# Performance work log

Hardware: AMD Instinct MI355X
Metric: run time of the kernel (lower is better)

The kernel has to match this reference:

```python
import jax, jax.numpy as jnp
import numpy as np

B, T, C, H, N = 4, 4096, 2048, 32, 64
DMIX, DDEC = 32, 64
N_LAYER, LAYER_ID = 24, 12
GN_EPS = 1e-5 * 8.0 ** 2  # eps = 1e-5 * head_size_divisor**2


def setup_inputs() -> dict:
    key = jax.random.key(0)
    ks = jax.random.split(key, 24)
    r01 = LAYER_ID / (N_LAYER - 1)
    r1a0 = 1.0 - LAYER_ID / N_LAYER
    ddd = (np.arange(C, dtype=np.float32) / C).reshape(1, 1, C)
    maa = lambda p: jnp.asarray(1.0 - ddd ** p, dtype=jnp.float32)
    # decay speed schedule (canonical RWKV6, over channel dim)
    n = np.arange(C, dtype=np.float32)
    decay = (-6.0 + 5.0 * (n / (C - 1)) ** (0.7 + 1.3 * r01)).reshape(1, 1, C)
    # time_faaaa zigzag schedule
    m = np.arange(C, dtype=np.float32)
    zig = ((m + 1) % 3 - 1) * 0.1
    faaaa = (r01 * (1 - m / (C - 1)) + zig).reshape(H, N)
    s = 1.0 / np.sqrt(C)
    return {
        "x": jax.random.normal(ks[0], (B, T, C), jnp.float32),
        "shift_state": jax.random.normal(ks[1], (B, C), jnp.float32),
        "wkv_state": jnp.zeros((B, H, N, N), jnp.float32),
        "time_maa_x": maa(r1a0),
        "time_maa_w": maa(r1a0),
        "time_maa_k": maa(r1a0),
        "time_maa_v": jnp.asarray(1.0 - (ddd ** r1a0 + 0.3 * r01), jnp.float32),
        "time_maa_r": maa(0.5 * r1a0),
        "time_maa_g": maa(0.5 * r1a0),
        "time_maa_w1": jax.random.normal(ks[2], (C, 5 * DMIX), jnp.float32) * 0.01,
        "time_maa_w2": jax.random.uniform(ks[3], (5, DMIX, C), jnp.float32, -0.01, 0.01),
        "time_decay": jnp.asarray(decay, jnp.float32),
        "time_decay_w1": jax.random.normal(ks[4], (C, DDEC), jnp.float32) * 0.01,
        "time_decay_w2": jax.random.uniform(ks[5], (DDEC, C), jnp.float32, -0.01, 0.01),
        "time_faaaa": jnp.asarray(faaaa, jnp.float32),
        "Wr": jax.random.normal(ks[6], (C, C), jnp.float32) * s,
        "Wk": jax.random.normal(ks[7], (C, C), jnp.float32) * s,
        "Wv": jax.random.normal(ks[8], (C, C), jnp.float32) * s,
        "Wg": jax.random.normal(ks[9], (C, C), jnp.float32) * s,
        "Wo": jax.random.normal(ks[10], (C, C), jnp.float32) * s,
        "gn_weight": jnp.ones((C,), jnp.float32),
        "gn_bias": jnp.zeros((C,), jnp.float32),
    }


def reference(x, shift_state, wkv_state, time_maa_x, time_maa_w, time_maa_k,
              time_maa_v, time_maa_r, time_maa_g, time_maa_w1, time_maa_w2,
              time_decay, time_decay_w1, time_decay_w2, time_faaaa,
              Wr, Wk, Wv, Wg, Wo, gn_weight, gn_bias):
    b, t, c = x.shape
    # token shift: previous token (seeded by shift_state) minus current
    xx = jnp.concatenate([shift_state[:, None, :], x[:, :-1]], axis=1) - x
    lx = x[:, -1]
    # LoRA token-shift mixing
    xxx = x + xx * time_maa_x
    t5 = jnp.tanh(xxx @ time_maa_w1).reshape(b, t, 5, DMIX)
    mixes = jnp.einsum('btfd,fdc->fbtc', t5, time_maa_w2)
    mw, mk, mv, mr, mg = mixes
    xw = x + xx * (time_maa_w + mw)
    xk = x + xx * (time_maa_k + mk)
    xv = x + xx * (time_maa_v + mv)
    xr = x + xx * (time_maa_r + mr)
    xg = x + xx * (time_maa_g + mg)
    r = xr @ Wr
    k = xk @ Wk
    v = xv @ Wv
    g = jax.nn.silu(xg @ Wg)
    # data-dependent decay via LoRA; wkv6 uses log-decay -exp(w)
    w = time_decay + jnp.tanh(xw @ time_decay_w1) @ time_decay_w2
    glog = -jnp.exp(w)  # [b,t,c]
    to_heads = lambda z: z.reshape(b, t, H, N).transpose(1, 0, 2, 3)  # [t,b,h,n]
    rh, kh, vh, gh = to_heads(r), to_heads(k), to_heads(v), to_heads(glog)
    u = time_faaaa  # [H,N]

    def step(S, inp):
        r_t, k_t, v_t, g_t = inp  # each [b,h,n]
        kv = jnp.einsum('bhk,bhv->bhkv', k_t, v_t)
        o_t = jnp.einsum('bhk,bhkv->bhv', r_t, S + u[None, :, :, None] * kv)
        S = jnp.exp(g_t)[..., None] * S + kv
        return S, o_t

    state, o = jax.lax.scan(step, wkv_state, (rh, kh, vh, gh))
    o = o.transpose(1, 0, 2, 3).reshape(b, t, c)  # [b,t,c]
    # GroupNorm with H groups over channel dim
    og = o.reshape(b, t, H, N)
    mu = og.mean(-1, keepdims=True)
    var = og.var(-1, keepdims=True)
    on = (og - mu) * jax.lax.rsqrt(var + GN_EPS)
    on = on * gn_weight.reshape(H, N) + gn_bias.reshape(H, N)
    out = (on.reshape(b, t, c) * g) @ Wo
    return out, lx, state
```

## Files before the change

kernel.cpp:

```cpp
#include <hip/hip_runtime.h>
#include <hip/hip_bf16.h>
#include <stdint.h>

#define DEV __device__ __forceinline__

typedef __bf16 bf16x8 __attribute__((ext_vector_type(8)));
typedef float f32x4 __attribute__((ext_vector_type(4)));
typedef unsigned short u16x8 __attribute__((ext_vector_type(8)));

constexpr int kB = 4, kT = 4096, kC = 2048, kH = 32, kN = 64;
constexpr int kM = kB * kT;
constexpr int SEGN = 8, TSEG = kT / SEGN, CHN = TSEG / 64;

DEV float bfu2f(unsigned short u) {
  union { uint32_t i; float f; } x; x.i = ((uint32_t)u) << 16; return x.f;
}
DEV unsigned short f2bfu(float f) {
  union { float f; uint32_t i; } x; x.f = f;
  uint32_t r = x.i + 0x7FFFu + ((x.i >> 16) & 1u);
  return (unsigned short)(r >> 16);
}

DEV void gld16(const void* g, void* l) {
  __builtin_amdgcn_global_load_lds(
      (const __attribute__((address_space(1))) void*)g,
      (__attribute__((address_space(3))) void*)l, 16, 0, 0);
}

DEV int swzb(int row, int byteoff) { return (row << 7) + (byteoff ^ ((row & 7) << 4)); }
DEV int swz64(int row, int byteoff) { return (row << 6) + (byteoff ^ ((row & 3) << 4)); }

__global__ __launch_bounds__(256) void trans_bf16(
    const float* __restrict__ in, unsigned short* __restrict__ out, int R, int Cn) {
  __shared__ __attribute__((aligned(16))) unsigned short tile[64][65];
  const int t = threadIdx.x;
  const int r0 = blockIdx.y * 64, c0 = blockIdx.x * 64;
  const int lr = t >> 6, lc = t & 63;
#pragma unroll
  for (int i = 0; i < 16; i++) {
    int rr = lr + i * 4;
    int gr = r0 + rr, gc = c0 + lc;
    if (gr < R && gc < Cn) tile[rr][lc] = f2bfu(in[(size_t)gr * Cn + gc]);
  }
  __syncthreads();
#pragma unroll
  for (int i = 0; i < 16; i++) {
    int cc = lr + i * 4;
    int gc = c0 + cc, gr = r0 + lc;
    if (gc < Cn && gr < R) out[(size_t)gc * R + gr] = tile[lc][cc];
  }
}

__global__ __launch_bounds__(256) void prep_x2(
    const float* __restrict__ x, const float* __restrict__ shift,
    const float* __restrict__ maax,
    unsigned short* __restrict__ xxx, float* __restrict__ lx) {
  size_t i4 = ((size_t)blockIdx.x * 256 + threadIdx.x) * 4;
  int c = (int)(i4 & (kC - 1));
  size_t bt = i4 >> 11;
  int tt = (int)(bt & (kT - 1));
  int b = (int)(bt >> 12);
  float4 xv = *(const float4*)(x + i4);
  float4 pv = (tt == 0) ? *(const float4*)(shift + (size_t)b * kC + c)
                        : *(const float4*)(x + i4 - kC);
  float4 mx = *(const float4*)(maax + c);
  ushort4 o4;
  o4.x = f2bfu(xv.x + (pv.x - xv.x) * mx.x);
  o4.y = f2bfu(xv.y + (pv.y - xv.y) * mx.y);
  o4.z = f2bfu(xv.z + (pv.z - xv.z) * mx.z);
  o4.w = f2bfu(xv.w + (pv.w - xv.w) * mx.w);
  *(ushort4*)(xxx + i4) = o4;
  if (tt == kT - 1) *(float4*)(lx + (size_t)b * kC + c) = xv;
}

enum { E_F32 = 0, E_BF16 = 1, E_TANH = 2, E_SILU = 3, E_DECAY = 4 };

template <int BM, int BN, int EPI>
__global__ __launch_bounds__(256) void gemm_k(
    const unsigned short* __restrict__ A, const unsigned short* __restrict__ Bt,
    void* __restrict__ Cout, const float* __restrict__ aux, int M, int N, int K) {
  constexpr int WGM = (BM == 128 && BN == 128) ? 2 : (BM == 64 ? 2 : 4);
  constexpr int WGN = 4 / WGM;
  constexpr int WM = BM / WGM, WN = BN / WGN;
  constexpr int WR = WM / 16, WC = WN / 16;
  __shared__ __attribute__((aligned(16))) unsigned short As[BM * 32];
  __shared__ __attribute__((aligned(16))) unsigned short Bs[BN * 32];
  const int t = threadIdx.x, wid = t >> 6, l = t & 63;
  const int m0 = blockIdx.x * BM, n0 = blockIdx.y * BN;
  const int wm0 = (wid / WGN) * WM, wn0 = (wid % WGN) * WN;
  f32x4 acc[WR][WC];
#pragma unroll
  for (int i = 0; i < WR; i++)
#pragma unroll
    for (int j = 0; j < WC; j++) acc[i][j] = f32x4{0.f, 0.f, 0.f, 0.f};

  const int rowS = t >> 2, cbS = (t & 3) * 16;
  const char* Ab = (const char*)A;
  const char* Bb = (const char*)Bt;
  const int aoff = (wm0 + (l & 15)) * 32 + (l >> 4) * 8;
  const int boff = (wn0 + (l & 15)) * 32 + (l >> 4) * 8;

  for (int kt = 0; kt < K; kt += 32) {
#pragma unroll
    for (int ia = 0; ia < BM / 64; ia++)
      gld16(Ab + ((size_t)(m0 + ia * 64 + rowS) * K + kt) * 2 + cbS,
            (char*)As + ia * 4096 + wid * 1024);
    if constexpr (BN >= 64) {
#pragma unroll
      for (int ib = 0; ib < BN / 64; ib++)
        gld16(Bb + ((size_t)(n0 + ib * 64 + rowS) * K + kt) * 2 + cbS,
              (char*)Bs + ib * 4096 + wid * 1024);
    } else {
      if (t < BN * 4)
        gld16(Bb + ((size_t)(n0 + rowS) * K + kt) * 2 + cbS,
              (char*)Bs + wid * 1024);
    }
    __syncthreads();
    bf16x8 af[WR], bfv[WC];
#pragma unroll
    for (int mi = 0; mi < WR; mi++) af[mi] = *(const bf16x8*)(&As[aoff + mi * 512]);
#pragma unroll
    for (int ni = 0; ni < WC; ni++) bfv[ni] = *(const bf16x8*)(&Bs[boff + ni * 512]);
#pragma unroll
    for (int mi = 0; mi < WR; mi++)
#pragma unroll
      for (int ni = 0; ni < WC; ni++)
        acc[mi][ni] = __builtin_amdgcn_mfma_f32_16x16x32_bf16(af[mi], bfv[ni], acc[mi][ni], 0, 0, 0);
    __syncthreads();
  }

#pragma unroll
  for (int mi = 0; mi < WR; mi++) {
#pragma unroll
    for (int ni = 0; ni < WC; ni++) {
      int row = m0 + wm0 + mi * 16 + (l >> 4) * 4;
      int col = n0 + wn0 + ni * 16 + (l & 15);
#pragma unroll
      for (int j = 0; j < 4; j++) {
        float v = acc[mi][ni][j];
        size_t idx = (size_t)(row + j) * N + col;
        if constexpr (EPI == E_F32) ((float*)Cout)[idx] = v;
        else if constexpr (EPI == E_BF16) ((unsigned short*)Cout)[idx] = f2bfu(v);
        else if constexpr (EPI == E_TANH) ((unsigned short*)Cout)[idx] = f2bfu(tanhf(v));
        else if constexpr (EPI == E_SILU) ((unsigned short*)Cout)[idx] = f2bfu(v / (1.f + expf(-v)));
        else if constexpr (EPI == E_DECAY) {
          float w = v + aux[col];
          ((float*)Cout)[idx] = expf(-expf(w));
        }
      }
    }
  }
}

template <int EPI>
__global__ __launch_bounds__(512, 2) void gemm256_k(
    const unsigned short* __restrict__ A, const unsigned short* __restrict__ Bt,
    void* __restrict__ Cout, int M, int N, int K) {
  extern __shared__ __attribute__((aligned(16))) char lds[];
  const int tid = threadIdx.x, wid = tid >> 6, l = tid & 63;
  const int fr = l & 15, fq = l >> 4;

  const int mtiles = M >> 8, ntiles = N >> 8;
  const int slab = mtiles >> 3;
  const int xcd = blockIdx.x & 7, loc = blockIdx.x >> 3;
  const int m0 = (xcd * slab + loc / ntiles) * 256;
  const int n0 = (loc % ntiles) * 256;

  const int wm = (wid >> 2) * 128, wn = (wid & 3) * 64;

  const int srow0 = tid >> 2;
  const int scb = ((tid & 3) * 16) ^ ((srow0 & 3) << 4);
  const char* pa2[2]; const char* pb2[2];
#pragma unroll
  for (int i = 0; i < 2; i++) {
    pa2[i] = (const char*)A + (size_t)(m0 + i * 128 + srow0) * K * 2 + scb;
    pb2[i] = (const char*)Bt + (size_t)(n0 + i * 128 + srow0) * K * 2 + scb;
  }

  const char* vA[8]; const char* vB[4];
#pragma unroll
  for (int mi = 0; mi < 8; mi++)
    vA[mi] = lds + swz64(wm + mi * 16 + fr, fq * 16);
#pragma unroll
  for (int ni = 0; ni < 4; ni++)
    vB[ni] = lds + 32768 + swz64(wn + ni * 16 + fr, fq * 16);

  f32x4 acc[8][4];
#pragma unroll
  for (int i = 0; i < 8; i++)
#pragma unroll
    for (int j = 0; j < 4; j++) acc[i][j] = f32x4{0.f, 0.f, 0.f, 0.f};

  auto STG = [&](int q, int s, int ktb) {
    const int d = q * 65536 + s * 16384 + wid * 1024;
    gld16(pa2[0] + ktb + s * 64, lds + d);
    gld16(pa2[1] + ktb + s * 64, lds + d + 8192);
    gld16(pb2[0] + ktb + s * 64, lds + 32768 + d);
    gld16(pb2[1] + ktb + s * 64, lds + 32768 + d + 8192);
  };

  auto PH = [&](int p, int s, bool doStage, int ktbNext, int vm) {
// ... 3 lines not shown
      asm volatile("s_waitcnt vmcnt(0)" ::: "memory");
    __builtin_amdgcn_s_barrier();
    __builtin_amdgcn_sched_barrier(0);
    const int pb = p * 65536 + s * 16384;
    bf16x8 a[8], b[4];
#pragma unroll
    for (int mi = 0; mi < 8; mi++) a[mi] = *(const bf16x8*)(vA[mi] + pb);
#pragma unroll
    for (int ni = 0; ni < 4; ni++) b[ni] = *(const bf16x8*)(vB[ni] + pb);
    if (doStage) STG(p ^ 1, s, ktbNext);
    __builtin_amdgcn_sched_barrier(0);
    __builtin_amdgcn_s_setprio(1);
#pragma unroll
    for (int ni = 0; ni < 4; ni++)
#pragma unroll
      for (int mi = 0; mi < 8; mi++)
        acc[mi][ni] = __builtin_amdgcn_mfma_f32_16x16x32_bf16(a[mi], b[ni], acc[mi][ni], 0, 0, 0);
    __builtin_amdgcn_s_setprio(0);
  };

  const int KT = K >> 6;
  STG(0, 0, 0);
  STG(0, 1, 0);

  int T = 0;
  for (; T + 2 < KT; T += 2) {
    PH(0, 0, true, (T + 1) * 128, 4);
    PH(0, 1, true, (T + 1) * 128, 4);
    PH(1, 0, true, (T + 2) * 128, 4);
    PH(1, 1, true, (T + 2) * 128, 4);
  }
  PH(0, 0, true, (KT - 1) * 128, 4);
  PH(0, 1, true, (KT - 1) * 128, 4);
  PH(1, 0, false, 0, 4);
  PH(1, 1, false, 0, 0);

#pragma unroll
  for (int mi = 0; mi < 8; mi++)
#pragma unroll
    for (int ni = 0; ni < 4; ni++) {
      int row = m0 + wm + mi * 16 + fq * 4;
      int col = n0 + wn + ni * 16 + fr;
#pragma unroll
      for (int j = 0; j < 4; j++) {
        float v = acc[mi][ni][j];
        size_t idx = (size_t)(row + j) * N + col;
        if constexpr (EPI == E_F32) ((float*)Cout)[idx] = v;
        else if constexpr (EPI == E_BF16) ((unsigned short*)Cout)[idx] = f2bfu(v);
        else if constexpr (EPI == E_SILU) ((unsigned short*)Cout)[idx] = f2bfu(v / (1.f + expf(-v)));
      }
    }
}

__global__ __launch_bounds__(256) void mix2f_k(
    const unsigned short* __restrict__ t5, const unsigned short* __restrict__ w2t,
    const float* __restrict__ x, const float* __restrict__ shift,
    const float* __restrict__ maa1, const float* __restrict__ maa2,
    unsigned short* __restrict__ xo1, unsigned short* __restrict__ xo2,
    int f1, int f2) {
  __shared__ __attribute__((aligned(16))) unsigned short As1[64 * 32];
  __shared__ __attribute__((aligned(16))) unsigned short Bs1[64 * 32];
  __shared__ __attribute__((aligned(16))) unsigned short As2[64 * 32];
  __shared__ __attribute__((aligned(16))) unsigned short Bs2[64 * 32];
  const int t = threadIdx.x, wid = t >> 6, l = t & 63;
  const int m0 = blockIdx.x * 64, n0 = blockIdx.y * 64;
  const int wm0 = (wid >> 1) * 32, wn0 = (wid & 1) * 32;
  const int rowS = t >> 2, cbS = (t & 3) * 16;
  const int aoff = (wm0 + (l & 15)) * 32 + (l >> 4) * 8;
  const int boff = (wn0 + (l & 15)) * 32 + (l >> 4) * 8;

  gld16((const char*)t5 + ((size_t)(m0 + rowS) * 160 + f1 * 32) * 2 + cbS, (char*)As1 + wid * 1024);
  gld16((const char*)w2t + ((size_t)(n0 + rowS) * 160 + f1 * 32) * 2 + cbS, (char*)Bs1 + wid * 1024);
  gld16((const char*)t5 + ((size_t)(m0 + rowS) * 160 + f2 * 32) * 2 + cbS, (char*)As2 + wid * 1024);
  gld16((const char*)w2t + ((size_t)(n0 + rowS) * 160 + f2 * 32) * 2 + cbS, (char*)Bs2 + wid * 1024);
  __syncthreads();
  bf16x8 a10 = *(const bf16x8*)(&As1[aoff]), a11 = *(const bf16x8*)(&As1[aoff + 512]);
  bf16x8 b10 = *(const bf16x8*)(&Bs1[boff]), b11 = *(const bf16x8*)(&Bs1[boff + 512]);
  bf16x8 a20 = *(const bf16x8*)(&As2[aoff]), a21 = *(const bf16x8*)(&As2[aoff + 512]);
  bf16x8 b20 = *(const bf16x8*)(&Bs2[boff]), b21 = *(const bf16x8*)(&Bs2[boff + 512]);
  f32x4 ac1[2][2], ac2[2][2];
#pragma unroll
  for (int i = 0; i < 2; i++)
#pragma unroll
    for (int j = 0; j < 2; j++) { ac1[i][j] = f32x4{0.f, 0.f, 0.f, 0.f}; ac2[i][j] = f32x4{0.f, 0.f, 0.f, 0.f}; }
  ac1[0][0] = __builtin_amdgcn_mfma_f32_16x16x32_bf16(a10, b10, ac1[0][0], 0, 0, 0);
  ac1[0][1] = __builtin_amdgcn_mfma_f32_16x16x32_bf16(a10, b11, ac1[0][1], 0, 0, 0);
  ac1[1][0] = __builtin_amdgcn_mfma_f32_16x16x32_bf16(a11, b10, ac1[1][0], 0, 0, 0);
  ac1[1][1] = __builtin_amdgcn_mfma_f32_16x16x32_bf16(a11, b11, ac1[1][1], 0, 0, 0);
  ac2[0][0] = __builtin_amdgcn_mfma_f32_16x16x32_bf16(a20, b20, ac2[0][0], 0, 0, 0);
  ac2[0][1] = __builtin_amdgcn_mfma_f32_16x16x32_bf16(a20, b21, ac2[0][1], 0, 0, 0);
  ac2[1][0] = __builtin_amdgcn_mfma_f32_16x16x32_bf16(a21, b20, ac2[1][0], 0, 0, 0);
  ac2[1][1] = __builtin_amdgcn_mfma_f32_16x16x32_bf16(a21, b21, ac2[1][1], 0, 0, 0);

#pragma unroll
  for (int mi = 0; mi < 2; mi++)
#pragma unroll
    for (int ni = 0; ni < 2; ni++) {
      int row = m0 + wm0 + mi * 16 + (l >> 4) * 4;
      int col = n0 + wn0 + ni * 16 + (l & 15);
      float mv1 = maa1[col], mv2 = maa2[col];
#pragma unroll
      for (int j = 0; j < 4; j++) {
        int rrow = row + j;
        int tt = rrow & (kT - 1);
        size_t idx = (size_t)rrow * kC + col;
        float xv = x[idx];
        float pv = (tt == 0) ? shift[(size_t)(rrow >> 12) * kC + col] : x[idx - kC];
        float d = pv - xv;
        xo1[idx] = f2bfu(xv + d * (mv1 + ac1[mi][ni][j]));
        xo2[idx] = f2bfu(xv + d * (mv2 + ac2[mi][ni][j]));
      }
    }
}

__global__ __launch_bounds__(256) void mixf_k(
    const unsigned short* __restrict__ t5, const unsigned short* __restrict__ w2t,
    const float* __restrict__ x, const float* __restrict__ shift,
    const float* __restrict__ maa, unsigned short* __restrict__ xout, int f) {
  __shared__ __attribute__((aligned(16))) unsigned short As[64 * 32];
  __shared__ __attribute__((aligned(16))) unsigned short Bs[64 * 32];
  const int t = threadIdx.x, wid = t >> 6, l = t & 63;
  const int m0 = blockIdx.x * 64, n0 = blockIdx.y * 64;
  const int wm0 = (wid >> 1) * 32, wn0 = (wid & 1) * 32;
  const int rowS = t >> 2, cbS = (t & 3) * 16;
  const int aoff = (wm0 + (l & 15)) * 32 + (l >> 4) * 8;
  const int boff = (wn0 + (l & 15)) * 32 + (l >> 4) * 8;

  gld16((const char*)t5 + ((size_t)(m0 + rowS) * 160 + f * 32) * 2 + cbS, (char*)As + wid * 1024);
  gld16((const char*)w2t + ((size_t)(n0 + rowS) * 160 + f * 32) * 2 + cbS, (char*)Bs + wid * 1024);
  __syncthreads();
  bf16x8 a0 = *(const bf16x8*)(&As[aoff]), a1 = *(const bf16x8*)(&As[aoff + 512]);
  bf16x8 b0 = *(const bf16x8*)(&Bs[boff]), b1 = *(const bf16x8*)(&Bs[boff + 512]);
  f32x4 acc[2][2];
  acc[0][0] = f32x4{0.f, 0.f, 0.f, 0.f}; acc[0][1] = f32x4{0.f, 0.f, 0.f, 0.f};
  acc[1][0] = f32x4{0.f, 0.f, 0.f, 0.f}; acc[1][1] = f32x4{0.f, 0.f, 0.f, 0.f};
  acc[0][0] = __builtin_amdgcn_mfma_f32_16x16x32_bf16(a0, b0, acc[0][0], 0, 0, 0);
  acc[0][1] = __builtin_amdgcn_mfma_f32_16x16x32_bf16(a0, b1, acc[0][1], 0, 0, 0);
  acc[1][0] = __builtin_amdgcn_mfma_f32_16x16x32_bf16(a1, b0, acc[1][0], 0, 0, 0);
  acc[1][1] = __builtin_amdgcn_mfma_f32_16x16x32_bf16(a1, b1, acc[1][1], 0, 0, 0);

#pragma unroll
  for (int mi = 0; mi < 2; mi++)
#pragma unroll
    for (int ni = 0; ni < 2; ni++) {
      int row = m0 + wm0 + mi * 16 + (l >> 4) * 4;
      int col = n0 + wn0 + ni * 16 + (l & 15);
      float mv = maa[col];
#pragma unroll
      for (int j = 0; j < 4; j++) {
        int rrow = row + j;
        int tt = rrow & (kT - 1);
        size_t idx = (size_t)rrow * kC + col;
        float xv = x[idx];
        float pv = (tt == 0) ? shift[(size_t)(rrow >> 12) * kC + col] : x[idx - kC];
        xout[idx] = f2bfu(xv + (pv - xv) * (mv + acc[mi][ni][j]));
      }
    }
}

__global__ __launch_bounds__(256) void wkv_local_k(
    const unsigned short* __restrict__ kb, const unsigned short* __restrict__ vb,
    const float* __restrict__ ed, float* __restrict__ Lbuf, float* __restrict__ Dseg) {
  const int bid = blockIdx.x;
  const int bh = bid >> 3, seg = bid & 7;
  const int h = bh & 31, b = bh >> 5;
  const int tid = threadIdx.x, w = tid >> 6, l = tid & 63;
  __shared__ __attribute__((aligned(16))) unsigned short KQks[4096];
  __shared__ __attribute__((aligned(16))) unsigned short Vt[4096];
  __shared__ float segp[4][64];
  __shared__ float DLs[64];

  const int fr = l & 15, fq = l >> 4;
  f32x4 Sreg[4];
#pragma unroll
  for (int ni = 0; ni < 4; ni++) Sreg[ni] = f32x4{0.f, 0.f, 0.f, 0.f};

  float dtot = 1.f;
  float kv[16], dv[16], vv[16];
  {
    size_t g = ((size_t)b * kT + seg * TSEG + w * 16) * kC + h * 64 + l;
#pragma unroll
    for (int i = 0; i < 16; i++) {
      kv[i] = bfu2f(kb[g]); vv[i] = bfu2f(vb[g]); dv[i] = ed[g];
      g += kC;
    }
  }

  for (int ch = 0; ch < CHN; ++ch) {
    float p = 1.f;
#pragma unroll
    for (int i = 0; i < 16; i++) p *= dv[i];
    segp[w][l] = p;
    __syncthreads();
    float pre = 1.f;
    if (w > 0) pre *= segp[0][l];
    if (w > 1) pre *= segp[1][l];
    if (w > 2) pre *= segp[2][l];
    if (w == 3) DLs[l] = pre * p;

    unsigned short kqrow[16], vtrow[16];
    float run = pre;
#pragma unroll
    for (int i = 0; i < 16; i++) {
      run *= dv[i];
      kqrow[i] = f2bfu(kv[i] / run);
      vtrow[i] = f2bfu(vv[i]);
    }
    {
      u16x8 q0, q1, v0, v1;
#pragma unroll
      for (int j = 0; j < 8; j++) { q0[j] = kqrow[j]; q1[j] = kqrow[j + 8]; v0[j] = vtrow[j]; v1[j] = vtrow[j + 8]; }
      *(u16x8*)((char*)KQks + swzb(l, w * 32)) = q0;
      *(u16x8*)((char*)KQks + swzb(l, w * 32 + 16)) = q1;
      *(u16x8*)((char*)Vt + swzb(l, w * 32)) = v0;
      *(u16x8*)((char*)Vt + swzb(l, w * 32 + 16)) = v1;
    }
    if (ch < CHN - 1) {
      size_t g = ((size_t)b * kT + seg * TSEG + (ch + 1) * 64 + w * 16) * kC + h * 64 + l;
#pragma unroll
      for (int i = 0; i < 16; i++) {
        kv[i] = bfu2f(kb[g]); vv[i] = bfu2f(vb[g]); dv[i] = ed[g];
        g += kC;
      }
    }
    __syncthreads();

    bf16x8 kA0 = *(const bf16x8*)((const char*)KQks + swzb(w * 16 + fr, fq * 16));
    bf16x8 kA1 = *(const bf16x8*)((const char*)KQks + swzb(w * 16 + fr, fq * 16 + 64));
    f32x4 kvacc[4];
#pragma unroll
    for (int ni = 0; ni < 4; ni++) {
      bf16x8 bv0 = *(const bf16x8*)((const char*)Vt + swzb(ni * 16 + fr, fq * 16));
      bf16x8 bv1 = *(const bf16x8*)((const char*)Vt + swzb(ni * 16 + fr, fq * 16 + 64));
      kvacc[ni] = __builtin_amdgcn_mfma_f32_16x16x32_bf16(kA0, bv0, f32x4{0.f, 0.f, 0.f, 0.f}, 0, 0, 0);
      kvacc[ni] = __builtin_amdgcn_mfma_f32_16x16x32_bf16(kA1, bv1, kvacc[ni], 0, 0, 0);
    }
    float dlj[4];
#pragma unroll
    for (int j = 0; j < 4; j++) dlj[j] = DLs[w * 16 + fq * 4 + j];
#pragma unroll
    for (int ni = 0; ni < 4; ni++)
#pragma unroll
      for (int j = 0; j < 4; j++)
        Sreg[ni][j] = (Sreg[ni][j] + kvacc[ni][j]) * dlj[j];
    dtot *= DLs[l];
    __syncthreads();
  }

  float* Lp = Lbuf + (size_t)bid * 4096;
#pragma unroll
  for (int ni = 0; ni < 4; ni++)
#pragma unroll
    for (int j = 0; j < 4; j++)
      Lp[(size_t)(w * 16 + fq * 4 + j) * 64 + ni * 16 + fr] = Sreg[ni][j];
  if (w == 0) Dseg[(size_t)bid * 64 + l] = dtot;
}

__global__ __launch_bounds__(256) void wkv_combine_k(
    const float* __restrict__ s0, const float* __restrict__ Dseg,
    float* __restrict__ Lbuf, float* __restrict__ sOut) {
  const int bh = blockIdx.x, tid = threadIdx.x;
  const int k = tid >> 2, v0 = (tid & 3) * 16;
  float4 s[4];
  const float* sp = s0 + (size_t)bh * 4096 + (size_t)k * 64 + v0;
#pragma unroll
  for (int q = 0; q < 4; q++) s[q] = ((const float4*)sp)[q];
  for (int seg = 0; seg < SEGN; ++seg) {
    size_t idx = (size_t)bh * SEGN + seg;
    float d = Dseg[idx * 64 + k];
    float* Lp = Lbuf + idx * 4096 + (size_t)k * 64 + v0;
#pragma unroll
    for (int q = 0; q < 4; q++) {
      float4 lq = ((float4*)Lp)[q];
      ((float4*)Lp)[q] = s[q];
      s[q].x = d * s[q].x + lq.x; s[q].y = d * s[q].y + lq.y;
      s[q].z = d * s[q].z + lq.z; s[q].w = d * s[q].w + lq.w;
    }
  }
  float* op = sOut + (size_t)bh * 4096 + (size_t)k * 64 + v0;
#pragma unroll
  for (int q = 0; q < 4; q++) ((float4*)op)[q] = s[q];
}

__global__ __launch_bounds__(256) void wkv_seg_k(
    const unsigned short* __restrict__ rb, const unsigned short* __restrict__ kb,
    const unsigned short* __restrict__ vb, const float* __restrict__ ed,
    const float* __restrict__ uf, const float* __restrict__ Sini,
    unsigned short* __restrict__ o) {
  const int bid = blockIdx.x;
  const int bh = bid >> 3, seg = bid & 7;
  const int h = bh & 31, b = bh >> 5;
  const int tid = threadIdx.x, w = tid >> 6, l = tid & 63;
  __shared__ __attribute__((aligned(16))) unsigned short RQ[4096];
  __shared__ __attribute__((aligned(16))) unsigned short KQsk[4096];
  __shared__ __attribute__((aligned(16))) unsigned short KQks[4096];
  __shared__ __attribute__((aligned(16))) unsigned short Vt[4096];
  __shared__ __attribute__((aligned(16))) unsigned short Pl[4096];
  __shared__ __attribute__((aligned(16))) unsigned short S0T[4096];
  __shared__ __attribute__((aligned(16))) unsigned short RU[4096];
// ... 95 lines not shown
    }
    float dg[4];
#pragma unroll
    for (int j = 0; j < 4; j++) dg[j] = __shfl(dacc[j], fq * 20 + j, 64);
#pragma unroll
    for (int ni = 0; ni < 4; ni++)
#pragma unroll
      for (int j = 0; j < 4; j++) {
        int row = w * 16 + fq * 4 + j, col = ni * 16 + fr;
        float pv = pacc[ni][j];
        pv = (col < row) ? pv : ((col == row) ? dg[j] : 0.f);
        *(unsigned short*)((char*)Pl + swzb(row, col * 2)) = f2bfu(pv);
      }
    __syncthreads();

    bf16x8 pA0 = *(const bf16x8*)((const char*)Pl + swzb(w * 16 + fr, fq * 16));
    bf16x8 pA1 = *(const bf16x8*)((const char*)Pl + swzb(w * 16 + fr, fq * 16 + 64));
    bf16x8 kA0 = *(const bf16x8*)((const char*)KQks + swzb(w * 16 + fr, fq * 16));
    bf16x8 kA1 = *(const bf16x8*)((const char*)KQks + swzb(w * 16 + fr, fq * 16 + 64));
    f32x4 oacc[4], kvacc[4];
#pragma unroll
    for (int ni = 0; ni < 4; ni++) {
      bf16x8 bv0 = *(const bf16x8*)((const char*)Vt + swzb(ni * 16 + fr, fq * 16));
      bf16x8 bv1 = *(const bf16x8*)((const char*)Vt + swzb(ni * 16 + fr, fq * 16 + 64));
      bf16x8 bs0 = *(const bf16x8*)((const char*)S0T + swzb(ni * 16 + fr, fq * 16));
      bf16x8 bs1 = *(const bf16x8*)((const char*)S0T + swzb(ni * 16 + fr, fq * 16 + 64));
      oacc[ni] = __builtin_amdgcn_mfma_f32_16x16x32_bf16(pA0, bv0, f32x4{0.f, 0.f, 0.f, 0.f}, 0, 0, 0);
      oacc[ni] = __builtin_amdgcn_mfma_f32_16x16x32_bf16(pA1, bv1, oacc[ni], 0, 0, 0);
      oacc[ni] = __builtin_amdgcn_mfma_f32_16x16x32_bf16(a0, bs0, oacc[ni], 0, 0, 0);
      oacc[ni] = __builtin_amdgcn_mfma_f32_16x16x32_bf16(a1, bs1, oacc[ni], 0, 0, 0);
      kvacc[ni] = __builtin_amdgcn_mfma_f32_16x16x32_bf16(kA0, bv0, f32x4{0.f, 0.f, 0.f, 0.f}, 0, 0, 0);
      kvacc[ni] = __builtin_amdgcn_mfma_f32_16x16x32_bf16(kA1, bv1, kvacc[ni], 0, 0, 0);
    }
    size_t obase = ((size_t)b * kT + seg * TSEG + ch * 64) * kC + h * 64;
#pragma unroll
    for (int ni = 0; ni < 4; ni++)
#pragma unroll
      for (int j = 0; j < 4; j++)
        o[obase + (size_t)(w * 16 + fq * 4 + j) * kC + ni * 16 + fr] = f2bfu(oacc[ni][j]);
    __syncthreads();

    float dlj[4];
#pragma unroll
    for (int j = 0; j < 4; j++) dlj[j] = DLs[w * 16 + fq * 4 + j];
#pragma unroll
    for (int ni = 0; ni < 4; ni++)
#pragma unroll
      for (int j = 0; j < 4; j++) {
        int kk2 = w * 16 + fq * 4 + j, vv2 = ni * 16 + fr;
        float sn = (Sreg[ni][j] + kvacc[ni][j]) * dlj[j];
        Sreg[ni][j] = sn;
        *(unsigned short*)((char*)S0T + swzb(vv2, kk2 * 2)) = f2bfu(sn);
      }
    __syncthreads();
  }
}

__global__ __launch_bounds__(256) void gn_k(
    const unsigned short* __restrict__ o, const unsigned short* __restrict__ gb,
    const float* __restrict__ gnw, const float* __restrict__ gnb,
    unsigned short* __restrict__ y) {
  int gi = blockIdx.x * 4 + (threadIdx.x >> 6);
  int j = threadIdx.x & 63;
  int bt = gi >> 5, h = gi & 31;
  size_t idx = (size_t)bt * kC + h * 64 + j;
  float val = bfu2f(o[idx]);
  float s = val, s2 = val * val;
#pragma unroll
  for (int m = 1; m < 64; m <<= 1) {
    s += __shfl_xor(s, m, 64);
    s2 += __shfl_xor(s2, m, 64);
  }
  float mu = s * 0.015625f;
  float var = s2 * 0.015625f - mu * mu;
  float rs = rsqrtf(var + 6.4e-4f);
  float on = (val - mu) * rs * gnw[h * 64 + j] + gnb[h * 64 + j];
  y[idx] = f2bfu(on * bfu2f(gb[idx]));
}

constexpr size_t SZW     = (size_t)2048 * 2048 * 2;
constexpr size_t OFF_WRT = 0;
constexpr size_t OFF_WKT = 1 * SZW;
constexpr size_t OFF_WVT = 2 * SZW;
constexpr size_t OFF_WGT = 3 * SZW;
constexpr size_t OFF_WOT = 4 * SZW;
constexpr size_t OFF_W1T = 5 * SZW;
constexpr size_t OFF_W2T = OFF_W1T + (size_t)160 * 2048 * 2;
constexpr size_t OFF_TD1 = OFF_W2T + (size_t)2048 * 160 * 2;
constexpr size_t OFF_TD2 = OFF_TD1 + (size_t)64 * 2048 * 2;
constexpr size_t OFF_T5  = OFF_TD2 + (size_t)2048 * 64 * 2;
constexpr size_t OFF_DT  = OFF_T5 + (size_t)kM * 160 * 2;
constexpr size_t OFF_EDEC= OFF_DT + (size_t)kM * 64 * 2;
constexpr size_t OFF_XMIX= OFF_EDEC + (size_t)kM * kC * 4;
constexpr size_t OFF_R   = OFF_XMIX + (size_t)kM * kC * 2;
constexpr size_t OFF_K   = OFF_R + (size_t)kM * kC * 2;
constexpr size_t OFF_V   = OFF_K + (size_t)kM * kC * 2;
constexpr size_t OFF_L   = OFF_WRT;

extern "C" void kernel_launch(void* const* d_in, const int* in_sizes, int n_in,
                              void* d_out, int out_size, void* d_ws, size_t ws_size,
                              hipStream_t stream) {
  const float* x     = (const float*)d_in[0];
  const float* shift = (const float*)d_in[1];
  const float* s0    = (const float*)d_in[2];
  const float* maax  = (const float*)d_in[3];
  const float* maaw  = (const float*)d_in[4];
  const float* maak  = (const float*)d_in[5];
  const float* maav  = (const float*)d_in[6];
  const float* maar  = (const float*)d_in[7];
  const float* maag  = (const float*)d_in[8];
  const float* w1    = (const float*)d_in[9];
  const float* w2    = (const float*)d_in[10];
  const float* tdec  = (const float*)d_in[11];
  const float* tdw1  = (const float*)d_in[12];
  const float* tdw2  = (const float*)d_in[13];
  const float* faaaa = (const float*)d_in[14];
  const float* Wr    = (const float*)d_in[15];
  const float* Wk    = (const float*)d_in[16];
  const float* Wv    = (const float*)d_in[17];
  const float* Wg    = (const float*)d_in[18];
  const float* Wo    = (const float*)d_in[19];
  const float* gnw   = (const float*)d_in[20];
  const float* gnb   = (const float*)d_in[21];

  char* ws = (char*)d_ws;
  unsigned short* Wrt  = (unsigned short*)(ws + OFF_WRT);
  unsigned short* Wkt  = (unsigned short*)(ws + OFF_WKT);
  unsigned short* Wvt  = (unsigned short*)(ws + OFF_WVT);
  unsigned short* Wgt  = (unsigned short*)(ws + OFF_WGT);
  unsigned short* Wot  = (unsigned short*)(ws + OFF_WOT);
  unsigned short* w1t  = (unsigned short*)(ws + OFF_W1T);
  unsigned short* w2t  = (unsigned short*)(ws + OFF_W2T);
  unsigned short* td1t = (unsigned short*)(ws + OFF_TD1);
  unsigned short* td2t = (unsigned short*)(ws + OFF_TD2);
  unsigned short* t5   = (unsigned short*)(ws + OFF_T5);
  unsigned short* dtmp = (unsigned short*)(ws + OFF_DT);
  float*          edec = (float*)(ws + OFF_EDEC);
  unsigned short* xg   = (unsigned short*)(ws + OFF_EDEC);
  unsigned short* bufX = (unsigned short*)(ws + OFF_XMIX);
  unsigned short* bufR = (unsigned short*)(ws + OFF_R);
  unsigned short* bufK = (unsigned short*)(ws + OFF_K);
  unsigned short* bufV = (unsigned short*)(ws + OFF_V);
  float*          Lbuf = (float*)(ws + OFF_L);
  float*          DsegP= (float*)(ws + OFF_TD1);

  float* outp  = (float*)d_out;
  float* lx    = outp + (size_t)kM * kC;
  float* stOut = lx + (size_t)kB * kC;

  dim3 blk(256);

  trans_bf16<<<dim3(32, 32), blk, 0, stream>>>(Wr, Wrt, 2048, 2048);
  trans_bf16<<<dim3(32, 32), blk, 0, stream>>>(Wk, Wkt, 2048, 2048);
  trans_bf16<<<dim3(32, 32), blk, 0, stream>>>(Wv, Wvt, 2048, 2048);
  trans_bf16<<<dim3(32, 32), blk, 0, stream>>>(Wg, Wgt, 2048, 2048);
  trans_bf16<<<dim3(32, 32), blk, 0, stream>>>(Wo, Wot, 2048, 2048);
  trans_bf16<<<dim3(3, 32), blk, 0, stream>>>(w1, w1t, 2048, 160);
  trans_bf16<<<dim3(1, 32), blk, 0, stream>>>(tdw1, td1t, 2048, 64);
  trans_bf16<<<dim3(32, 1), blk, 0, stream>>>(tdw2, td2t, 64, 2048);
  trans_bf16<<<dim3(32, 3), blk, 0, stream>>>(w2, w2t, 160, 2048);

  prep_x2<<<dim3(kM * kC / 4 / 256), blk, 0, stream>>>(x, shift, maax, bufX, lx);

  gemm_k<128, 32, E_TANH><<<dim3(kM / 128, 5), blk, 0, stream>>>(bufX, w1t, t5, nullptr, kM, 160, 2048);

  dim3 mgrid(kM / 64, kC / 64);
  constexpr int G256 = (kM / 256) * (kC / 256);
  constexpr size_t LDS256 = 131072;

  mix2f_k<<<mgrid, blk, 0, stream>>>(t5, w2t, x, shift, maaw, maak, bufX, bufV, 0, 1);
  gemm_k<64, 64, E_TANH><<<dim3(kM / 64, 1), blk, 0, stream>>>(bufX, td1t, dtmp, nullptr, kM, 64, 2048);
  gemm_k<128, 128, E_DECAY><<<dim3(kM / 128, 16), blk, 0, stream>>>(dtmp, td2t, edec, tdec, kM, 2048, 64);
  gemm256_k<E_BF16><<<dim3(G256), dim3(512), LDS256, stream>>>(bufV, Wkt, bufK, kM, 2048, 2048);

  mix2f_k<<<mgrid, blk, 0, stream>>>(t5, w2t, x, shift, maav, maar, bufX, bufV, 2, 3);
  gemm256_k<E_BF16><<<dim3(G256), dim3(512), LDS256, stream>>>(bufX, Wvt, bufR, kM, 2048, 2048);
  gemm256_k<E_BF16><<<dim3(G256), dim3(512), LDS256, stream>>>(bufV, Wrt, bufX, kM, 2048, 2048);

  wkv_local_k<<<dim3(kB * kH * SEGN), blk, 0, stream>>>(bufK, bufR, edec, Lbuf, DsegP);
  wkv_combine_k<<<dim3(kB * kH), blk, 0, stream>>>(s0, DsegP, Lbuf, stOut);
  wkv_seg_k<<<dim3(kB * kH * SEGN), blk, 0, stream>>>(bufX, bufK, bufR, edec, faaaa, Lbuf, bufV);

  mixf_k<<<mgrid, blk, 0, stream>>>(t5, w2t, x, shift, maag, xg, 4);
  gemm256_k<E_SILU><<<dim3(G256), dim3(512), LDS256, stream>>>(xg, Wgt, bufK, kM, 2048, 2048);

  gn_k<<<dim3(kM * kH / 4), blk, 0, stream>>>(bufV, bufK, gnw, gnb, bufR);

  gemm256_k<E_F32><<<dim3(G256), dim3(512), LDS256, stream>>>(bufR, Wot, outp, kM, 2048, 2048);
}
```

Baseline: 1.522 ms.

## Fuse decay LoRA second GEMM into wkv_local and merge four token-mix kernels

The separate decay GEMM, which wrote the full fp32 decay tensor, is removed. wkv_local now computes exp(-exp(dtmp@td2 + time_decay)) per chunk with MFMA from LDS, writes it to edec for the later segment kernel, and uses it directly. The two mix2f launches become one mix4f that produces the w/k/v/r mixes in a single pass over x, and buffers are reassigned. This drops one large kernel, one full reread of the decay tensor and one extra pass over x and shift, at the cost of more LDS and extra work inside the wkv kernel. Two trailing syncthreads are also removed.

```diff
diff --git a/kernel.cpp b/kernel.cpp
--- a/kernel.cpp
+++ b/kernel.cpp
@@ -73,12 +73,12 @@
   if (tt == kT - 1) *(float4*)(lx + (size_t)b * kC + c) = xv;
 }
 
-enum { E_F32 = 0, E_BF16 = 1, E_TANH = 2, E_SILU = 3, E_DECAY = 4 };
+enum { E_F32 = 0, E_BF16 = 1, E_TANH = 2, E_SILU = 3 };
 
 template <int BM, int BN, int EPI>
 __global__ __launch_bounds__(256) void gemm_k(
     const unsigned short* __restrict__ A, const unsigned short* __restrict__ Bt,
-    void* __restrict__ Cout, const float* __restrict__ aux, int M, int N, int K) {
+    void* __restrict__ Cout, int M, int N, int K) {
   constexpr int WGM = (BM == 128 && BN == 128) ? 2 : (BM == 64 ? 2 : 4);
   constexpr int WGN = 4 / WGM;
   constexpr int WM = BM / WGM, WN = BN / WGN;
@@ -143,10 +143,6 @@
         else if constexpr (EPI == E_BF16) ((unsigned short*)Cout)[idx] = f2bfu(v);
         else if constexpr (EPI == E_TANH) ((unsigned short*)Cout)[idx] = f2bfu(tanhf(v));
         else if constexpr (EPI == E_SILU) ((unsigned short*)Cout)[idx] = f2bfu(v / (1.f + expf(-v)));
-        else if constexpr (EPI == E_DECAY) {
-          float w = v + aux[col];
-          ((float*)Cout)[idx] = expf(-expf(w));
-        }
       }
     }
   }
@@ -256,16 +252,15 @@
     }
 }
 
-__global__ __launch_bounds__(256) void mix2f_k(
+__global__ __launch_bounds__(256) void mix4f_k(
     const unsigned short* __restrict__ t5, const unsigned short* __restrict__ w2t,
     const float* __restrict__ x, const float* __restrict__ shift,
-    const float* __restrict__ maa1, const float* __restrict__ maa2,
-    unsigned short* __restrict__ xo1, unsigned short* __restrict__ xo2,
-    int f1, int f2) {
-  __shared__ __attribute__((aligned(16))) unsigned short As1[64 * 32];
-  __shared__ __attribute__((aligned(16))) unsigned short Bs1[64 * 32];
-  __shared__ __attribute__((aligned(16))) unsigned short As2[64 * 32];
-  __shared__ __attribute__((aligned(16))) unsigned short Bs2[64 * 32];
+    const float* __restrict__ maaw, const float* __restrict__ maak,
+    const float* __restrict__ maav, const float* __restrict__ maar,
+    unsigned short* __restrict__ xw, unsigned short* __restrict__ xk,
+    unsigned short* __restrict__ xv, unsigned short* __restrict__ xr) {
+  __shared__ __attribute__((aligned(16))) unsigned short As[4][64 * 32];
+  __shared__ __attribute__((aligned(16))) unsigned short Bs[4][64 * 32];
   const int t = threadIdx.x, wid = t >> 6, l = t & 63;
   const int m0 = blockIdx.x * 64, n0 = blockIdx.y * 64;
   const int wm0 = (wid >> 1) * 32, wn0 = (wid & 1) * 32;
@@ -273,28 +268,22 @@
   const int aoff = (wm0 + (l & 15)) * 32 + (l >> 4) * 8;
   const int boff = (wn0 + (l & 15)) * 32 + (l >> 4) * 8;
 
-  gld16((const char*)t5 + ((size_t)(m0 + rowS) * 160 + f1 * 32) * 2 + cbS, (char*)As1 + wid * 1024);
-  gld16((const char*)w2t + ((size_t)(n0 + rowS) * 160 + f1 * 32) * 2 + cbS, (char*)Bs1 + wid * 1024);
-  gld16((const char*)t5 + ((size_t)(m0 + rowS) * 160 + f2 * 32) * 2 + cbS, (char*)As2 + wid * 1024);
-  gld16((const char*)w2t + ((size_t)(n0 + rowS) * 160 + f2 * 32) * 2 + cbS, (char*)Bs2 + wid * 1024);
+#pragma unroll
+  for (int f = 0; f < 4; f++) {
+    gld16((const char*)t5 + ((size_t)(m0 + rowS) * 160 + f * 32) * 2 + cbS, (char*)As[f] + wid * 1024);
+    gld16((const char*)w2t + ((size_t)(n0 + rowS) * 160 + f * 32) * 2 + cbS, (char*)Bs[f] + wid * 1024);
+  }
   __syncthreads();
-  bf16x8 a10 = *(const bf16x8*)(&As1[aoff]), a11 = *(const bf16x8*)(&As1[aoff + 512]);
-  bf16x8 b10 = *(const bf16x8*)(&Bs1[boff]), b11 = *(const bf16x8*)(&Bs1[boff + 512]);
-  bf16x8 a20 = *(const bf16x8*)(&As2[aoff]), a21 = *(const bf16x8*)(&As2[aoff + 512]);
-  bf16x8 b20 = *(const bf16x8*)(&Bs2[boff]), b21 = *(const bf16x8*)(&Bs2[boff + 512]);
-  f32x4 ac1[2][2], ac2[2][2];
-#pragma unroll
-  for (int i = 0; i < 2; i++)
-#pragma unroll
-    for (int j = 0; j < 2; j++) { ac1[i][j] = f32x4{0.f, 0.f, 0.f, 0.f}; ac2[i][j] = f32x4{0.f, 0.f, 0.f, 0.f}; }
-  ac1[0][0] = __builtin_amdgcn_mfma_f32_16x16x32_bf16(a10, b10, ac1[0][0], 0, 0, 0);
-  ac1[0][1] = __builtin_amdgcn_mfma_f32_16x16x32_bf16(a10, b11, ac1[0][1], 0, 0, 0);
-  ac1[1][0] = __builtin_amdgcn_mfma_f32_16x16x32_bf16(a11, b10, ac1[1][0], 0, 0, 0);
-  ac1[1][1] = __builtin_amdgcn_mfma_f32_16x16x32_bf16(a11, b11, ac1[1][1], 0, 0, 0);
-  ac2[0][0] = __builtin_amdgcn_mfma_f32_16x16x32_bf16(a20, b20, ac2[0][0], 0, 0, 0);
-  ac2[0][1] = __builtin_amdgcn_mfma_f32_16x16x32_bf16(a20, b21, ac2[0][1], 0, 0, 0);
-  ac2[1][0] = __builtin_amdgcn_mfma_f32_16x16x32_bf16(a21, b20, ac2[1][0], 0, 0, 0);
-  ac2[1][1] = __builtin_amdgcn_mfma_f32_16x16x32_bf16(a21, b21, ac2[1][1], 0, 0, 0);
+  f32x4 ac[4][2][2];
+#pragma unroll
+  for (int f = 0; f < 4; f++) {
+    bf16x8 a0 = *(const bf16x8*)(&As[f][aoff]), a1 = *(const bf16x8*)(&As[f][aoff + 512]);
+    bf16x8 b0 = *(const bf16x8*)(&Bs[f][boff]), b1 = *(const bf16x8*)(&Bs[f][boff + 512]);
+    ac[f][0][0] = __builtin_amdgcn_mfma_f32_16x16x32_bf16(a0, b0, f32x4{0.f, 0.f, 0.f, 0.f}, 0, 0, 0);
+    ac[f][0][1] = __builtin_amdgcn_mfma_f32_16x16x32_bf16(a0, b1, f32x4{0.f, 0.f, 0.f, 0.f}, 0, 0, 0);
+    ac[f][1][0] = __builtin_amdgcn_mfma_f32_16x16x32_bf16(a1, b0, f32x4{0.f, 0.f, 0.f, 0.f}, 0, 0, 0);
+    ac[f][1][1] = __builtin_amdgcn_mfma_f32_16x16x32_bf16(a1, b1, f32x4{0.f, 0.f, 0.f, 0.f}, 0, 0, 0);
+  }
 
 #pragma unroll
   for (int mi = 0; mi < 2; mi++)
@@ -302,17 +291,19 @@
     for (int ni = 0; ni < 2; ni++) {
       int row = m0 + wm0 + mi * 16 + (l >> 4) * 4;
       int col = n0 + wn0 + ni * 16 + (l & 15);
-      float mv1 = maa1[col], mv2 = maa2[col];
+      float mw = maaw[col], mk = maak[col], mv = maav[col], mr = maar[col];
 #pragma unroll
       for (int j = 0; j < 4; j++) {
         int rrow = row + j;
         int tt = rrow & (kT - 1);
         size_t idx = (size_t)rrow * kC + col;
-        float xv = x[idx];
+        float xvv = x[idx];
         float pv = (tt == 0) ? shift[(size_t)(rrow >> 12) * kC + col] : x[idx - kC];
-        float d = pv - xv;
-        xo1[idx] = f2bfu(xv + d * (mv1 + ac1[mi][ni][j]));
-        xo2[idx] = f2bfu(xv + d * (mv2 + ac2[mi][ni][j]));
+        float d = pv - xvv;
+        xw[idx] = f2bfu(xvv + d * (mw + ac[0][mi][ni][j]));
+        xk[idx] = f2bfu(xvv + d * (mk + ac[1][mi][ni][j]));
+        xv[idx] = f2bfu(xvv + d * (mv + ac[2][mi][ni][j]));
+        xr[idx] = f2bfu(xvv + d * (mr + ac[3][mi][ni][j]));
       }
     }
 }
@@ -336,12 +327,10 @@
   bf16x8 a0 = *(const bf16x8*)(&As[aoff]), a1 = *(const bf16x8*)(&As[aoff + 512]);
   bf16x8 b0 = *(const bf16x8*)(&Bs[boff]), b1 = *(const bf16x8*)(&Bs[boff + 512]);
   f32x4 acc[2][2];
-  acc[0][0] = f32x4{0.f, 0.f, 0.f, 0.f}; acc[0][1] = f32x4{0.f, 0.f, 0.f, 0.f};
-  acc[1][0] = f32x4{0.f, 0.f, 0.f, 0.f}; acc[1][1] = f32x4{0.f, 0.f, 0.f, 0.f};
-  acc[0][0] = __builtin_amdgcn_mfma_f32_16x16x32_bf16(a0, b0, acc[0][0], 0, 0, 0);
-  acc[0][1] = __builtin_amdgcn_mfma_f32_16x16x32_bf16(a0, b1, acc[0][1], 0, 0, 0);
-  acc[1][0] = __builtin_amdgcn_mfma_f32_16x16x32_bf16(a1, b0, acc[1][0], 0, 0, 0);
-  acc[1][1] = __builtin_amdgcn_mfma_f32_16x16x32_bf16(a1, b1, acc[1][1], 0, 0, 0);
+  acc[0][0] = __builtin_amdgcn_mfma_f32_16x16x32_bf16(a0, b0, f32x4{0.f, 0.f, 0.f, 0.f}, 0, 0, 0);
+  acc[0][1] = __builtin_amdgcn_mfma_f32_16x16x32_bf16(a0, b1, f32x4{0.f, 0.f, 0.f, 0.f}, 0, 0, 0);
+  acc[1][0] = __builtin_amdgcn_mfma_f32_16x16x32_bf16(a1, b0, f32x4{0.f, 0.f, 0.f, 0.f}, 0, 0, 0);
+  acc[1][1] = __builtin_amdgcn_mfma_f32_16x16x32_bf16(a1, b1, f32x4{0.f, 0.f, 0.f, 0.f}, 0, 0, 0);
 
 #pragma unroll
   for (int mi = 0; mi < 2; mi++)
@@ -364,38 +353,94 @@
 
 __global__ __launch_bounds__(256) void wkv_local_k(
     const unsigned short* __restrict__ kb, const unsigned short* __restrict__ vb,
-    const float* __restrict__ ed, float* __restrict__ Lbuf, float* __restrict__ Dseg) {
+    const unsigned short* __restrict__ dtmp, const unsigned short* __restrict__ td2t,
+    const float* __restrict__ tdec,
+    float* __restrict__ Lbuf, float* __restrict__ Dseg, float* __restrict__ edec) {
   const int bid = blockIdx.x;
   const int bh = bid >> 3, seg = bid & 7;
   const int h = bh & 31, b = bh >> 5;
   const int tid = threadIdx.x, w = tid >> 6, l = tid & 63;
-  __shared__ __attribute__((aligned(16))) unsigned short KQks[4096];
-  __shared__ __attribute__((aligned(16))) unsigned short Vt[4096];
+  __shared__ __attribute__((aligned(16))) char arena[32768];
+  char* KQks = arena;
+  char* Vt   = arena + 8192;
+  float* EdB = (float*)arena;
+  char* TdB  = arena + 16384;
+  char* DtA  = arena + 24576;
   __shared__ float segp[4][64];
   __shared__ float DLs[64];
+  __shared__ float tdf[64];
 
   const int fr = l & 15, fq = l >> 4;
   f32x4 Sreg[4];
 #pragma unroll
   for (int ni = 0; ni < 4; ni++) Sreg[ni] = f32x4{0.f, 0.f, 0.f, 0.f};
 
+  {
+    int r1 = tid >> 3, r2 = 32 + r1;
+    int cb1 = ((tid & 7) * 16) ^ ((r1 & 7) << 4);
+    int cb2 = ((tid & 7) * 16) ^ ((r2 & 7) << 4);
+    gld16((const char*)td2t + (size_t)(h * 64 + r1) * 128 + cb1, TdB + w * 1024);
+    gld16((const char*)td2t + (size_t)(h * 64 + r2) * 128 + cb2, TdB + 4096 + w * 1024);
+    if (tid < 64) tdf[tid] = tdec[h * 64 + tid];
+  }
+
   float dtot = 1.f;
-  float kv[16], dv[16], vv[16];
+  float kv[16], vv[16];
   {
     size_t g = ((size_t)b * kT + seg * TSEG + w * 16) * kC + h * 64 + l;
 #pragma unroll
     for (int i = 0; i < 16; i++) {
-      kv[i] = bfu2f(kb[g]); vv[i] = bfu2f(vb[g]); dv[i] = ed[g];
+      kv[i] = bfu2f(kb[g]); vv[i] = bfu2f(vb[g]);
       g += kC;
     }
   }
 
   for (int ch = 0; ch < CHN; ++ch) {
+    const size_t gt0 = (size_t)b * kT + seg * TSEG + ch * 64;
+    {
+      int r1 = tid >> 3, r2 = 32 + r1;
+      int cb1 = ((tid & 7) * 16) ^ ((r1 & 7) << 4);
+      int cb2 = ((tid & 7) * 16) ^ ((r2 & 7) << 4);
+      gld16((const char*)dtmp + (gt0 + r1) * 128 + cb1, DtA + w * 1024);
+      gld16((const char*)dtmp + (gt0 + r2) * 128 + cb2, DtA + 4096 + w * 1024);
+    }
+    __syncthreads();
+
+    f32x4 dacc[4];
+    {
+      bf16x8 af0 = *(const bf16x8*)(DtA + swzb(w * 16 + fr, fq * 16));
+      bf16x8 af1 = *(const bf16x8*)(DtA + swzb(w * 16 + fr, fq * 16 + 64));
+#pragma unroll
+      for (int nj = 0; nj < 4; nj++) {
+        bf16x8 b0 = *(const bf16x8*)(TdB + swzb(nj * 16 + fr, fq * 16));
+        bf16x8 b1 = *(const bf16x8*)(TdB + swzb(nj * 16 + fr, fq * 16 + 64));
+        dacc[nj] = __builtin_amdgcn_mfma_f32_16x16x32_bf16(af0, b0, f32x4{0.f, 0.f, 0.f, 0.f}, 0, 0, 0);
+        dacc[nj] = __builtin_amdgcn_mfma_f32_16x16x32_bf16(af1, b1, dacc[nj], 0, 0, 0);
+      }
+    }
+#pragma unroll
+    for (int nj = 0; nj < 4; nj++) {
+      float tv = tdf[nj * 16 + fr];
+#pragma unroll
+      for (int j = 0; j < 4; j++)
+        EdB[(w * 16 + fq * 4 + j) * 64 + nj * 16 + fr] = expf(-expf(dacc[nj][j] + tv));
+    }
+    __syncthreads();
+
+    float dvv[16];
     float p = 1.f;
-#pragma unroll
-    for (int i = 0; i < 16; i++) p *= dv[i];
+    {
+      size_t eg = (gt0 + w * 16) * kC + h * 64 + l;
+#pragma unroll
+      for (int i = 0; i < 16; i++) {
+        float d = EdB[(w * 16 + i) * 64 + l];
+        dvv[i] = d; p *= d;
+        edec[eg] = d; eg += kC;
+      }
+    }
     segp[w][l] = p;
     __syncthreads();
+
     float pre = 1.f;
     if (w > 0) pre *= segp[0][l];
     if (w > 1) pre *= segp[1][l];
@@ -406,7 +451,7 @@
     float run = pre;
 #pragma unroll
     for (int i = 0; i < 16; i++) {
-      run *= dv[i];
+      run *= dvv[i];
       kqrow[i] = f2bfu(kv[i] / run);
       vtrow[i] = f2bfu(vv[i]);
     }
@@ -414,28 +459,28 @@
       u16x8 q0, q1, v0, v1;
 #pragma unroll
       for (int j = 0; j < 8; j++) { q0[j] = kqrow[j]; q1[j] = kqrow[j + 8]; v0[j] = vtrow[j]; v1[j] = vtrow[j + 8]; }
-      *(u16x8*)((char*)KQks + swzb(l, w * 32)) = q0;
-      *(u16x8*)((char*)KQks + swzb(l, w * 32 + 16)) = q1;
-      *(u16x8*)((char*)Vt + swzb(l, w * 32)) = v0;
-      *(u16x8*)((char*)Vt + swzb(l, w * 32 + 16)) = v1;
+      *(u16x8*)(KQks + swzb(l, w * 32)) = q0;
+      *(u16x8*)(KQks + swzb(l, w * 32 + 16)) = q1;
+      *(u16x8*)(Vt + swzb(l, w * 32)) = v0;
+      *(u16x8*)(Vt + swzb(l, w * 32 + 16)) = v1;
     }
     if (ch < CHN - 1) {
       size_t g = ((size_t)b * kT + seg * TSEG + (ch + 1) * 64 + w * 16) * kC + h * 64 + l;
 #pragma unroll
       for (int i = 0; i < 16; i++) {
-        kv[i] = bfu2f(kb[g]); vv[i] = bfu2f(vb[g]); dv[i] = ed[g];
+        kv[i] = bfu2f(kb[g]); vv[i] = bfu2f(vb[g]);
         g += kC;
       }
     }
     __syncthreads();
 
-    bf16x8 kA0 = *(const bf16x8*)((const char*)KQks + swzb(w * 16 + fr, fq * 16));
-    bf16x8 kA1 = *(const bf16x8*)((const char*)KQks + swzb(w * 16 + fr, fq * 16 + 64));
+    bf16x8 kA0 = *(const bf16x8*)(KQks + swzb(w * 16 + fr, fq * 16));
+    bf16x8 kA1 = *(const bf16x8*)(KQks + swzb(w * 16 + fr, fq * 16 + 64));
     f32x4 kvacc[4];
 #pragma unroll
     for (int ni = 0; ni < 4; ni++) {
-      bf16x8 bv0 = *(const bf16x8*)((const char*)Vt + swzb(ni * 16 + fr, fq * 16));
-      bf16x8 bv1 = *(const bf16x8*)((const char*)Vt + swzb(ni * 16 + fr, fq * 16 + 64));
+      bf16x8 bv0 = *(const bf16x8*)(Vt + swzb(ni * 16 + fr, fq * 16));
+      bf16x8 bv1 = *(const bf16x8*)(Vt + swzb(ni * 16 + fr, fq * 16 + 64));
       kvacc[ni] = __builtin_amdgcn_mfma_f32_16x16x32_bf16(kA0, bv0, f32x4{0.f, 0.f, 0.f, 0.f}, 0, 0, 0);
       kvacc[ni] = __builtin_amdgcn_mfma_f32_16x16x32_bf16(kA1, bv1, kvacc[ni], 0, 0, 0);
     }
@@ -448,7 +493,6 @@
       for (int j = 0; j < 4; j++)
         Sreg[ni][j] = (Sreg[ni][j] + kvacc[ni][j]) * dlj[j];
     dtot *= DLs[l];
-    __syncthreads();
   }
 
   float* Lp = Lbuf + (size_t)bid * 4096;
@@ -650,7 +694,6 @@
         Sreg[ni][j] = sn;
         *(unsigned short*)((char*)S0T + swzb(vv2, kk2 * 2)) = f2bfu(sn);
       }
-    __syncthreads();
   }
 }
 
@@ -689,8 +732,8 @@
 constexpr size_t OFF_T5  = OFF_TD2 + (size_t)2048 * 64 * 2;
 constexpr size_t OFF_DT  = OFF_T5 + (size_t)kM * 160 * 2;
 constexpr size_t OFF_EDEC= OFF_DT + (size_t)kM * 64 * 2;
-constexpr size_t OFF_XMIX= OFF_EDEC + (size_t)kM * kC * 4;
-constexpr size_t OFF_R   = OFF_XMIX + (size_t)kM * kC * 2;
+constexpr size_t OFF_X   = OFF_EDEC + (size_t)kM * kC * 4;
+constexpr size_t OFF_R   = OFF_X + (size_t)kM * kC * 2;
 constexpr size_t OFF_K   = OFF_R + (size_t)kM * kC * 2;
 constexpr size_t OFF_V   = OFF_K + (size_t)kM * kC * 2;
 constexpr size_t OFF_L   = OFF_WRT;
@@ -735,7 +778,7 @@
   unsigned short* dtmp = (unsigned short*)(ws + OFF_DT);
   float*          edec = (float*)(ws + OFF_EDEC);
   unsigned short* xg   = (unsigned short*)(ws + OFF_EDEC);
-  unsigned short* bufX = (unsigned short*)(ws + OFF_XMIX);
+  unsigned short* bufX = (unsigned short*)(ws + OFF_X);
   unsigned short* bufR = (unsigned short*)(ws + OFF_R);
   unsigned short* bufK = (unsigned short*)(ws + OFF_K);
   unsigned short* bufV = (unsigned short*)(ws + OFF_V);
@@ -760,29 +803,29 @@
 
   prep_x2<<<dim3(kM * kC / 4 / 256), blk, 0, stream>>>(x, shift, maax, bufX, lx);
 
-  gemm_k<128, 32, E_TANH><<<dim3(kM / 128, 5), blk, 0, stream>>>(bufX, w1t, t5, nullptr, kM, 160, 2048);
+  gemm_k<128, 32, E_TANH><<<dim3(kM / 128, 5), blk, 0, stream>>>(bufX, w1t, t5, kM, 160, 2048);
 
   dim3 mgrid(kM / 64, kC / 64);
   constexpr int G256 = (kM / 256) * (kC / 256);
   constexpr size_t LDS256 = 131072;
 
-  mix2f_k<<<mgrid, blk, 0, stream>>>(t5, w2t, x, shift, maaw, maak, bufX, bufV, 0, 1);
-  gemm_k<64, 64, E_TANH><<<dim3(kM / 64, 1), blk, 0, stream>>>(bufX, td1t, dtmp, nullptr, kM, 64, 2048);
-  gemm_k<128, 128, E_DECAY><<<dim3(kM / 128, 16), blk, 0, stream>>>(dtmp, td2t, edec, tdec, kM, 2048, 64);
-  gemm256_k<E_BF16><<<dim3(G256), dim3(512), LDS256, stream>>>(bufV, Wkt, bufK, kM, 2048, 2048);
-
-  mix2f_k<<<mgrid, blk, 0, stream>>>(t5, w2t, x, shift, maav, maar, bufX, bufV, 2, 3);
-  gemm256_k<E_BF16><<<dim3(G256), dim3(512), LDS256, stream>>>(bufX, Wvt, bufR, kM, 2048, 2048);
-  gemm256_k<E_BF16><<<dim3(G256), dim3(512), LDS256, stream>>>(bufV, Wrt, bufX, kM, 2048, 2048);
-
-  wkv_local_k<<<dim3(kB * kH * SEGN), blk, 0, stream>>>(bufK, bufR, edec, Lbuf, DsegP);
+  mix4f_k<<<mgrid, blk, 0, stream>>>(t5, w2t, x, shift, maaw, maak, maav, maar,
+                                     bufX, bufV, bufR, bufK);
+  gemm_k<64, 64, E_TANH><<<dim3(kM / 64, 1), blk, 0, stream>>>(bufX, td1t, dtmp, kM, 64, 2048);
+
+  gemm256_k<E_BF16><<<dim3(G256), dim3(512), LDS256, stream>>>(bufV, Wkt, bufX, kM, 2048, 2048);
+  gemm256_k<E_BF16><<<dim3(G256), dim3(512), LDS256, stream>>>(bufR, Wvt, bufV, kM, 2048, 2048);
+  gemm256_k<E_BF16><<<dim3(G256), dim3(512), LDS256, stream>>>(bufK, Wrt, bufR, kM, 2048, 2048);
+
+  wkv_local_k<<<dim3(kB * kH * SEGN), blk, 0, stream>>>(bufX, bufV, dtmp, td2t, tdec,
+                                                        Lbuf, DsegP, edec);
   wkv_combine_k<<<dim3(kB * kH), blk, 0, stream>>>(s0, DsegP, Lbuf, stOut);
-  wkv_seg_k<<<dim3(kB * kH * SEGN), blk, 0, stream>>>(bufX, bufK, bufR, edec, faaaa, Lbuf, bufV);
+  wkv_seg_k<<<dim3(kB * kH * SEGN), blk, 0, stream>>>(bufR, bufX, bufV, edec, faaaa, Lbuf, bufK);
 
   mixf_k<<<mgrid, blk, 0, stream>>>(t5, w2t, x, shift, maag, xg, 4);
-  gemm256_k<E_SILU><<<dim3(G256), dim3(512), LDS256, stream>>>(xg, Wgt, bufK, kM, 2048, 2048);
-
-  gn_k<<<dim3(kM * kH / 4), blk, 0, stream>>>(bufV, bufK, gnw, gnb, bufR);
-
-  gemm256_k<E_F32><<<dim3(G256), dim3(512), LDS256, stream>>>(bufR, Wot, outp, kM, 2048, 2048);
-}
+  gemm256_k<E_SILU><<<dim3(G256), dim3(512), LDS256, stream>>>(xg, Wgt, bufX, kM, 2048, 2048);
+
+  gn_k<<<dim3(kM * kH / 4), blk, 0, stream>>>(bufK, bufX, gnw, gnb, bufV);
+
+  gemm256_k<E_F32><<<dim3(G256), dim3(512), LDS256, stream>>>(bufV, Wot, outp, kM, 2048, 2048);
+}
```

Result: no change. 1.516 ms (-0.4%).
